# Performance work log

Hardware: AMD Instinct MI355X
Metric: run time of the kernel (lower is better)

## Reference

```python
import jax, jax.numpy as jnp
import numpy as np

B, M, D = 64, 256, 256          # batch, tokens, feature dim
A = 18                          # num_actions
E, S = 4, 64                    # num_experts, slots per expert (E*S == M)
H = 512                         # expert hidden size


def setup_inputs() -> dict:
    key = jax.random.key(0)
    ks = jax.random.split(key, 7)
    obs = jax.random.normal(ks[0], (B, M, D), dtype=jnp.float32)
    action = jax.random.randint(ks[1], (B,), 0, A, dtype=jnp.int64)
    # Soft-MoE slot projection phi: [D, E, S]
    phi = jax.random.normal(ks[2], (D, E, S), dtype=jnp.float32) / np.sqrt(D)
    # Per-expert MLP: Dense(H) + relu, then Dense(A*D) output head
    w1 = jax.random.normal(ks[3], (E, D, H), dtype=jnp.float32) * np.sqrt(2.0 / D)
    b1 = jnp.zeros((E, H), dtype=jnp.float32)
    w2 = jax.random.normal(ks[4], (E, H, A * D), dtype=jnp.float32) * np.sqrt(2.0 / H)
    b2 = jnp.zeros((E, A * D), dtype=jnp.float32)
    return {"obs": obs, "action": action, "phi": phi,
            "w1": w1, "b1": b1, "w2": w2, "b2": b2}


def reference(obs, action, phi, w1, b1, w2, b2):
    b, m, d = obs.shape
    # ---- Soft-MoE dispatch / combine (Puigcerver et al.) ----
    logits = jnp.einsum('bmd,des->bmes', obs, phi)            # [b,m,e,s]
    dispatch = jax.nn.softmax(logits, axis=1)                 # softmax over tokens
    combine = jax.nn.softmax(logits.reshape(b, m, E * S), axis=-1)
    combine = combine.reshape(b, m, E, S)                     # softmax over all slots
    slots = jnp.einsum('bmd,bmes->besd', obs, dispatch)       # [b,e,s,d]
    # ---- per-expert MLP: Dense(H)+relu -> Dense(A*d) ----
    h = jax.nn.relu(jnp.einsum('besd,edh->besh', slots, w1) + b1[None, :, None, :])
    y = jnp.einsum('besh,ehk->besk', h, w2) + b2[None, :, None, :]   # k = A*d
    # ---- combine slots back to tokens ----
    out = jnp.einsum('bmes,besk->bmk', combine, y)            # [b,m,A*d]
    # reshape to [b, A, m, d] as in the original module
    out = out.reshape(b, m, A, d).transpose(0, 2, 1, 3)       # [b,A,m,d]
    # ---- one-hot action selection via einsum (as in source) ----
    action_one_hot = jax.nn.one_hot(action, A, dtype=out.dtype)
    logits_out = jnp.einsum('bamd,ba->bmd', out, action_one_hot)
    return logits_out  # logits of the categorical transition distribution
```

## Files before the change

### kernel.cpp

```cpp
#include <hip/hip_runtime.h>

#define B_   64
#define M_   256
#define D_   256
#define A_   18
#define E_   4
#define S_   64
#define ES_  256
#define H_   512
#define K2_  (A_*D_)

typedef _Float16 f16;
typedef _Float16 f16x4 __attribute__((ext_vector_type(4)));
typedef _Float16 f16x8 __attribute__((ext_vector_type(8)));
typedef float    f32x4 __attribute__((ext_vector_type(4)));

static __device__ __forceinline__ f16x8 cat8(f16x4 a, f16x4 b) {
  return __builtin_shufflevector(a, b, 0, 1, 2, 3, 4, 5, 6, 7);
}
static __device__ __forceinline__ f16x8 pack8(float4 u0, float4 u1) {
  f16x8 a;
  a[0] = (f16)u0.x; a[1] = (f16)u0.y; a[2] = (f16)u0.z; a[3] = (f16)u0.w;
  a[4] = (f16)u1.x; a[5] = (f16)u1.y; a[6] = (f16)u1.z; a[7] = (f16)u1.w;
  return a;
}

typedef const __attribute__((address_space(1))) unsigned int guint;
typedef __attribute__((address_space(3))) unsigned int luint;
static __device__ __forceinline__ void gload16(const f16* g, f16* l) {
  __builtin_amdgcn_global_load_lds((guint*)g, (luint*)l, 16, 0, 0);
}
#define VMCNT(n)  asm volatile("s_waitcnt vmcnt(" #n ")" ::: "memory")
#define LGKMCNT0  asm volatile("s_waitcnt lgkmcnt(0)" ::: "memory")
#define SBAR()    __builtin_amdgcn_s_barrier()
#define SCHED0()  __builtin_amdgcn_sched_barrier(0)
#define MFMA16(a, b, c) __builtin_amdgcn_mfma_f32_16x16x32_f16(a, b, c, 0, 0, 0)

__global__ __launch_bounds__(256) void k_preplog(
    const float* __restrict__ obs, const float* __restrict__ phi,
    const float* __restrict__ w1, const float* __restrict__ w2,
    const int* __restrict__ action,
    f16* __restrict__ obsT16, f16* __restrict__ w1T, f16* __restrict__ w2T,
    int* __restrict__ order,
    f16* __restrict__ exp16, f16* __restrict__ expT16,
    float* __restrict__ rowpart, float* __restrict__ colpart)
{
  __shared__ f16 Bs[64][264];
  f16 (*T)[68] = reinterpret_cast<f16(*)[68]>(&Bs[0][0]);
  const int bx = blockIdx.x;
  const int t  = threadIdx.x;

  if (bx < 3456) {
    const int rr = t >> 4, cc = (t & 15) * 4;
    const float* src; f16* dst; int R, C, r0, c0;
    if (bx < 1024) {
      const int x = bx & 3, y = (bx >> 2) & 3, z = bx >> 4;
      src = obs + (long)z * (M_ * D_); dst = obsT16 + (long)z * (M_ * D_);
      R = M_; C = D_; r0 = y * 64; c0 = x * 64;
    } else if (bx < 1152) {
      const int idx = bx - 1024;
      const int x = idx & 7, y = (idx >> 3) & 3, z = idx >> 5;
      src = w1 + (long)z * (D_ * H_); dst = w1T + (long)z * (H_ * D_);
      R = D_; C = H_; r0 = y * 64; c0 = x * 64;
    } else {
      const int idx = bx - 1152;
      const int x = idx % 72, rem = idx / 72, y = rem & 7, z = rem >> 3;
      src = w2 + (long)z * ((long)H_ * K2_); dst = w2T + (long)z * ((long)K2_ * H_);
      R = H_; C = K2_; r0 = y * 64; c0 = x * 64;
    }
#pragma unroll
    for (int p = 0; p < 4; ++p) {
      const int row = rr + p * 16;
      const float4 v = *reinterpret_cast<const float4*>(
          &src[(long)(r0 + row) * C + c0 + cc]);
      f16x4 h4; h4[0] = (f16)v.x; h4[1] = (f16)v.y;
      h4[2] = (f16)v.z; h4[3] = (f16)v.w;
      *reinterpret_cast<f16x4*>(&T[row][cc]) = h4;
    }
    __syncthreads();
#pragma unroll
    for (int p = 0; p < 4; ++p) {
      const int oc = rr + p * 16;
      f16x4 g;
#pragma unroll
      for (int i = 0; i < 4; ++i) g[i] = T[cc + i][oc];
      *reinterpret_cast<f16x4*>(&dst[(long)(c0 + oc) * R + r0 + cc]) = g;
    }
    return;
  }

  if (bx == 3456) {
    if (t < B_) {
      const int a = action[t];
      int rank = 0;
#pragma unroll 8
      for (int i = 0; i < B_; ++i) {
        const int ai = action[i];
        rank += (ai < a) || (ai == a && i < t);
      }
      order[rank] = t;
    }
    return;
  }

  const int lb  = bx - 3457;
  const int es0 = (lb & 3) * 64, m0g = ((lb >> 2) & 3) * 64;
  const int bz  = lb >> 4;
  const long bo = (long)bz * (M_ * D_);
  const long bb = (long)bz * (M_ * ES_);

  {
    const int el = t & 63, wg = t >> 6;
#pragma unroll
    for (int dp = 0; dp < D_; dp += 32) {
      f16x8 hv;
#pragma unroll
      for (int j = 0; j < 8; ++j)
        hv[j] = (f16)phi[(long)(dp + wg * 8 + j) * ES_ + es0 + el];
      *reinterpret_cast<f16x8*>(&Bs[el][dp + wg * 8]) = hv;
    }
  }
  __syncthreads();

  const int w = t >> 6, lane = t & 63;
  const int wr = w >> 1, wc = w & 1;
  const int lr = lane & 15, lk = (lane >> 4) * 8;
  const int orow = (lane >> 4) * 4;

  f32x4 acc[2][2] = {};
  const float* Ap = obs + bo + (long)(m0g + wr * 32 + lr) * D_ + lk;
#pragma unroll
  for (int k0 = 0; k0 < D_; k0 += 32) {
    const float4 u00 = *reinterpret_cast<const float4*>(Ap + k0);
    const float4 u01 = *reinterpret_cast<const float4*>(Ap + k0 + 4);
    const float4 u10 = *reinterpret_cast<const float4*>(Ap + 16 * D_ + k0);
    const float4 u11 = *reinterpret_cast<const float4*>(Ap + 16 * D_ + k0 + 4);
    const f16x8 a0 = pack8(u00, u01);
    const f16x8 a1 = pack8(u10, u11);
    const f16x8 b0 = *reinterpret_cast<const f16x8*>(&Bs[wc * 32 + lr][k0 + lk]);
    const f16x8 b1 = *reinterpret_cast<const f16x8*>(&Bs[wc * 32 + 16 + lr][k0 + lk]);
    acc[0][0] = MFMA16(a0, b0, acc[0][0]);
    acc[0][1] = MFMA16(a0, b1, acc[0][1]);
    acc[1][0] = MFMA16(a1, b0, acc[1][0]);
    acc[1][1] = MFMA16(a1, b1, acc[1][1]);
  }
  __syncthreads();

#pragma unroll
  for (int fi = 0; fi < 2; ++fi)
#pragma unroll
    for (int fj = 0; fj < 2; ++fj) {
      const int gm = wr * 32 + fi * 16 + orow;
      const int gn = wc * 32 + fj * 16 + lr;
#pragma unroll
      for (int r = 0; r < 4; ++r)
        T[gm + r][gn] = (f16)__expf(acc[fi][fj][r]);
    }
  __syncthreads();

  {
    const int row = t >> 2, q = t & 3;
    f16x4 p0 = *reinterpret_cast<const f16x4*>(&T[row][q * 16 + 0]);
    f16x4 p1 = *reinterpret_cast<const f16x4*>(&T[row][q * 16 + 4]);
    f16x4 p2 = *reinterpret_cast<const f16x4*>(&T[row][q * 16 + 8]);
    f16x4 p3 = *reinterpret_cast<const f16x4*>(&T[row][q * 16 + 12]);
    f16* dst = exp16 + bb + (long)(m0g + row) * ES_ + es0 + q * 16;
    *reinterpret_cast<f16x8*>(dst)     = cat8(p0, p1);
    *reinterpret_cast<f16x8*>(dst + 8) = cat8(p2, p3);
  }
  {
    const int er = t >> 2, q = t & 3;
    f16x4 g[4];
#pragma unroll
    for (int j = 0; j < 4; ++j)
#pragma unroll
      for (int i = 0; i < 4; ++i)
        g[j][i] = T[q * 16 + j * 4 + i][er];
    f16* dst = expT16 + bb + (long)(es0 + er) * M_ + m0g + q * 16;
    *reinterpret_cast<f16x8*>(dst)     = cat8(g[0], g[1]);
    *reinterpret_cast<f16x8*>(dst + 8) = cat8(g[2], g[3]);
  }
  if (t < 64) {
    float s = 0.f;
#pragma unroll
    for (int i = 0; i < 16; ++i) {
      const f16x4 v = *reinterpret_cast<const f16x4*>(&T[t][i * 4]);
      s += (float)v[0] + (float)v[1] + (float)v[2] + (float)v[3];
    }
    rowpart[((long)bz * 256 + m0g + t) * 4 + (lb & 3)] = s;
  } else if (t < 128) {
    const int es = t - 64;
    float s = 0.f;
#pragma unroll
    for (int i = 0; i < 64; ++i) s += (float)T[i][es];
    colpart[((long)bz * 256 + es0 + es) * 4 + ((lb >> 2) & 3)] = s;
  }
}

__global__ __launch_bounds__(512, 4) void k_hy8(
    const f16* __restrict__ expT16, const f16* __restrict__ obsT16,
    const float* __restrict__ colpart,
    const f16* __restrict__ w1T, const float* __restrict__ b1,
    const f16* __restrict__ w2T, const float* __restrict__ b2,
    const int* __restrict__ action, const int* __restrict__ order,
    f16* __restrict__ yT16)
{
  __shared__ f16 lds[40960];
  f16* stg = lds;
  f16* ssO = lds + 16384;
  f16* hsO = lds + 24576;

  const int bx = blockIdx.x;
  const int L  = (bx & 7) * 64 + (bx >> 3);
  const int sb = L >> 3, e = (L >> 1) & 3, half = L & 1;
  const int b = order[sb];
  const int s0 = half * 32;
  int a = action[b];
  a = (a < 0) ? 0 : (a >= A_ ? A_ - 1 : a);

  const int t = threadIdx.x, w = t >> 6, lane = t & 63;
  const int lr = lane & 15, lk = (lane >> 4) * 8;
  const int seg = lane >> 4;
  const int orow = (lane >> 4) * 4;
  const int xorA = (lr & 7) << 3;

  const f16* srcB0 = obsT16 + (long)b * (D_ * M_);
  const f16* srcB1 = w1T + (long)e * (H_ * D_);
  const f16* srcB2 = w2T + (long)e * ((long)K2_ * H_) + (long)a * D_ * H_;
  const f16* ApG0  = expT16 + (long)b * (ES_ * M_)
                   + (long)(e * S_ + s0 + lr) * M_ + lk;

  f32x4 acc00 = {}, acc01 = {}, acc10 = {}, acc11 = {};
#pragma unroll 1
  for (int kt = 0; kt < 8; ++kt) {
    __syncthreads();
#pragma unroll
    for (int p = 0; p < 2; ++p) {
      const int j = (w * 2 + p) * 64 + lane;
      const int row = j >> 2, sg = (j & 3) ^ (row & 3);
      gload16(srcB0 + (long)row * M_ + kt * 32 + sg * 8, stg + (w * 2 + p) * 512);
    }
    __syncthreads();
    const f16x8 a0 = *reinterpret_cast<const f16x8*>(ApG0 + kt * 32);
    const f16x8 a1 = *reinterpret_cast<const f16x8*>(ApG0 + 16 * M_ + kt * 32);
    const int r0 = w * 32 + lr, r1 = w * 32 + 16 + lr;
    const f16x8 b0 = *reinterpret_cast<const f16x8*>(&stg[r0 * 32 + ((seg ^ (r0 & 3)) * 8)]);
    const f16x8 b1 = *reinterpret_cast<const f16x8*>(&stg[r1 * 32 + ((seg ^ (r1 & 3)) * 8)]);
    acc00 = MFMA16(a0, b0, acc00); acc01 = MFMA16(a0, b1, acc01);
    acc10 = MFMA16(a1, b0, acc10); acc11 = MFMA16(a1, b1, acc11);
  }
  __syncthreads();

#pragma unroll
  for (int p = 0; p < 4; ++p) {
    const int j = (w * 4 + p) * 64 + lane;
    const int row = j >> 2, sg = (j & 3) ^ (row & 3);
    gload16(srcB1 + (long)row * D_ + 0 * 32 + sg * 8, stg + (w * 4 + p) * 512);
  }
  {
    f32x4 accs[2][2] = {{acc00, acc01}, {acc10, acc11}};
    const int n0 = w * 32;
#pragma unroll
    for (int fi = 0; fi < 2; ++fi) {
      float inv[4];
#pragma unroll
      for (int r = 0; r < 4; ++r) {
        const int ges = e * S_ + s0 + fi * 16 + orow + r;
        const float4 cp = *reinterpret_cast<const float4*>(
            &colpart[((long)b * 256 + ges) * 4]);
        inv[r] = 1.0f / (cp.x + cp.y + cp.z + cp.w);
      }
#pragma unroll
      for (int fj = 0; fj < 2; ++fj) {
        const int gn = n0 + fj * 16 + lr;
#pragma unroll
        for (int r = 0; r < 4; ++r) {
          const int row = fi * 16 + orow + r;
          ssO[row * 256 + (gn ^ ((row & 7) << 3))] = (f16)(accs[fi][fj][r] * inv[r]);
        }
      }
    }
  }
#pragma unroll
  for (int p = 0; p < 4; ++p) {
    const int j = (w * 4 + p) * 64 + lane;
    const int row = j >> 2, sg = (j & 3) ^ (row & 3);
    gload16(srcB1 + (long)row * D_ + 1 * 32 + sg * 8, hsO + (w * 4 + p) * 512);
  }
  LGKMCNT0; SBAR(); SCHED0();

  f32x4 g1acc[2][4] = {};
#pragma unroll 1
  for (int kt = 0; kt < 7; ++kt) {
    VMCNT(4); SBAR(); SCHED0();
    f16* buf = (kt & 1) ? hsO : stg;
    {
      const f16x8 af0 = *reinterpret_cast<const f16x8*>(
          &ssO[lr * 256 + ((kt * 32 + lk) ^ xorA)]);
      const f16x8 af1 = *reinterpret_cast<const f16x8*>(
          &ssO[(16 + lr) * 256 + ((kt * 32 + lk) ^ xorA)]);
#pragma unroll
      for (int fj = 0; fj < 4; ++fj) {
        const int rB = w * 64 + fj * 16 + lr;
        const f16x8 bf = *reinterpret_cast<const f16x8*>(
            &buf[rB * 32 + ((seg ^ (rB & 3)) * 8)]);
        g1acc[0][fj] = MFMA16(af0, bf, g1acc[0][fj]);
        g1acc[1][fj] = MFMA16(af1, bf, g1acc[1][fj]);
      }
    }
    SBAR();
    if (kt < 6) {
#pragma unroll
      for (int p = 0; p < 4; ++p) {
        const int j = (w * 4 + p) * 64 + lane;
        const int row = j >> 2, sg = (j & 3) ^ (row & 3);
        gload16(srcB1 + (long)row * D_ + (kt + 2) * 32 + sg * 8, buf + (w * 4 + p) * 512);
      }
    }
  }
  VMCNT(0); SBAR(); SCHED0();
  {
    const f16x8 af0 = *reinterpret_cast<const f16x8*>(
        &ssO[lr * 256 + ((7 * 32 + lk) ^ xorA)]);
    const f16x8 af1 = *reinterpret_cast<const f16x8*>(
        &ssO[(16 + lr) * 256 + ((7 * 32 + lk) ^ xorA)]);
#pragma unroll
    for (int fj = 0; fj < 4; ++fj) {
      const int rB = w * 64 + fj * 16 + lr;
      const f16x8 bf = *reinterpret_cast<const f16x8*>(
          &hsO[rB * 32 + ((seg ^ (rB & 3)) * 8)]);
      g1acc[0][fj] = MFMA16(af0, bf, g1acc[0][fj]);
      g1acc[1][fj] = MFMA16(af1, bf, g1acc[1][fj]);
    }
  }
  SBAR();

#pragma unroll
  for (int p = 0; p < 2; ++p) {
    const int j = (w * 2 + p) * 64 + lane;
    const int row = j >> 2, sg = (j & 3) ^ (row & 3);
    gload16(srcB2 + (long)row * H_ + 0 * 32 + sg * 8, stg + (w * 2 + p) * 512);
  }
#pragma unroll
  for (int p = 0; p < 2; ++p) {
    const int j = (w * 2 + p) * 64 + lane;
    const int row = j >> 2, sg = (j & 3) ^ (row & 3);
    gload16(srcB2 + (long)row * H_ + 1 * 32 + sg * 8, stg + 8192 + (w * 2 + p) * 512);
  }
  {
    const int n1 = w * 64;
#pragma unroll
    for (int fi = 0; fi < 2; ++fi)
#pragma unroll
      for (int fj = 0; fj < 4; ++fj) {
        const int gn = n1 + fj * 16 + lr;
        const float bv = b1[e * H_ + gn];
#pragma unroll
        for (int r = 0; r < 4; ++r) {
          const int row = fi * 16 + orow + r;
          hsO[row * 512 + (gn ^ ((row & 7) << 3))] =
              (f16)fmaxf(g1acc[fi][fj][r] + bv, 0.f);
        }
      }
  }
  LGKMCNT0; SBAR(); SCHED0();

  f32x4 acc2[2][2] = {};
#pragma unroll 1
  for (int kt = 0; kt < 15; ++kt) {
    VMCNT(2); SBAR(); SCHED0();
    f16* buf = stg + (kt & 1) * 8192;
    {
      const f16x8 af0 = *reinterpret_cast<const f16x8*>(
          &hsO[lr * 512 + ((kt * 32 + lk) ^ xorA)]);
      const f16x8 af1 = *reinterpret_cast<const f16x8*>(
          &hsO[(16 + lr) * 512 + ((kt * 32 + lk) ^ xorA)]);
#pragma unroll
      for (int fj = 0; fj < 2; ++fj) {
        const int rB = w * 32 + fj * 16 + lr;
        const f16x8 bf = *reinterpret_cast<const f16x8*>(
            &buf[rB * 32 + ((seg ^ (rB & 3)) * 8)]);
        acc2[0][fj] = MFMA16(af0, bf, acc2[0][fj]);
        acc2[1][fj] = MFMA16(af1, bf, acc2[1][fj]);
      }
    }
    SBAR();
    if (kt < 14) {
#pragma unroll
      for (int p = 0; p < 2; ++p) {
        const int j = (w * 2 + p) * 64 + lane;
        const int row = j >> 2, sg = (j & 3) ^ (row & 3);
        gload16(srcB2 + (long)row * H_ + (kt + 2) * 32 + sg * 8, buf + (w * 2 + p) * 512);
      }
    }
  }
  VMCNT(0); SBAR(); SCHED0();
  {
    const f16x8 af0 = *reinterpret_cast<const f16x8*>(
        &hsO[lr * 512 + ((15 * 32 + lk) ^ xorA)]);
    const f16x8 af1 = *reinterpret_cast<const f16x8*>(
        &hsO[(16 + lr) * 512 + ((15 * 32 + lk) ^ xorA)]);
#pragma unroll
    for (int fj = 0; fj < 2; ++fj) {
      const int rB = w * 32 + fj * 16 + lr;
      const f16x8 bf = *reinterpret_cast<const f16x8*>(
          &stg[8192 + rB * 32 + ((seg ^ (rB & 3)) * 8)]);
      acc2[0][fj] = MFMA16(af0, bf, acc2[0][fj]);
      acc2[1][fj] = MFMA16(af1, bf, acc2[1][fj]);
    }
  }
  {
    const int n0_2 = w * 32;
#pragma unroll
    for (int fi = 0; fi < 2; ++fi)
#pragma unroll
      for (int fj = 0; fj < 2; ++fj) {
        const int gm = fi * 16 + orow;
        const int gn = n0_2 + fj * 16 + lr;
        const float bv = b2[e * K2_ + a * D_ + gn];
        f16x4 h4;
#pragma unroll
        for (int r = 0; r < 4; ++r) h4[r] = (f16)(acc2[fi][fj][r] + bv);
        *reinterpret_cast<f16x4*>(
            &yT16[(long)b * (D_ * ES_) + (long)gn * ES_ + e * S_ + s0 + gm]) = h4;
      }
  }
}

__global__ __launch_bounds__(256) void k_out_s(
    const f16* __restrict__ exp16, const f16* __restrict__ yT16,
    const float* __restrict__ rowpart, float* __restrict__ out)
{
  const int t = threadIdx.x;
  const int w = t >> 6, lane = t & 63;
  const int wr = w >> 1, wc = w & 1;
  const int m0 = blockIdx.y * 64 + wr * 32;
  const int n0 = blockIdx.x * 64 + wc * 32;
  const int lr = lane & 15, lk = (lane >> 4) * 8;
  const long b = blockIdx.z;

  f32x4 acc[2][2] = {};
  const f16* Ap = exp16 + b * (M_ * ES_) + (long)(m0 + lr) * ES_ + lk;
  const f16* Bp = yT16 + b * (D_ * ES_) + (long)(n0 + lr) * ES_ + lk;
#pragma unroll
  for (int k0 = 0; k0 < ES_; k0 += 32) {
    const f16x8 a0 = *reinterpret_cast<const f16x8*>(Ap + k0);
    const f16x8 a1 = *reinterpret_cast<const f16x8*>(Ap + 16 * ES_ + k0);
    const f16x8 b0 = *reinterpret_cast<const f16x8*>(Bp + k0);
    const f16x8 b1 = *reinterpret_cast<const f16x8*>(Bp + 16 * ES_ + k0);
    acc[0][0] = MFMA16(a0, b0, acc[0][0]);
    acc[0][1] = MFMA16(a0, b1, acc[0][1]);
    acc[1][0] = MFMA16(a1, b0, acc[1][0]);
    acc[1][1] = MFMA16(a1, b1, acc[1][1]);
  }

  const int orow = (lane >> 4) * 4;
  float* C = out + b * (M_ * D_);
#pragma unroll
  for (int fi = 0; fi < 2; ++fi) {
    float inv[4];
#pragma unroll
    for (int r = 0; r < 4; ++r) {
      const int gm = m0 + fi * 16 + orow + r;
      const float4 rp = *reinterpret_cast<const float4*>(&rowpart[((long)b * 256 + gm) * 4]);
      inv[r] = 1.0f / (rp.x + rp.y + rp.z + rp.w);
    }
#pragma unroll
    for (int fj = 0; fj < 2; ++fj) {
      const int gm = m0 + fi * 16 + orow;
      const int gn = n0 + fj * 16 + lr;
#pragma unroll
      for (int r = 0; r < 4; ++r)
        C[(long)(gm + r) * D_ + gn] = acc[fi][fj][r] * inv[r];
    }
  }
}

extern "C" void kernel_launch(void* const* d_in, const int* in_sizes, int n_in,
                              void* d_out, int out_size, void* d_ws, size_t ws_size,
                              hipStream_t stream)
{
  const float* obs    = (const float*)d_in[0];
  const int*   action = (const int*)d_in[1];
  const float* phi    = (const float*)d_in[2];
  const float* w1     = (const float*)d_in[3];
  const float* b1     = (const float*)d_in[4];
  const float* w2     = (const float*)d_in[5];
  const float* b2     = (const float*)d_in[6];
  float*       out    = (float*)d_out;

  f16* ws = (f16*)d_ws;
  f16* obsT16  = ws + 0;
  f16* w1T     = ws + 4194304;
  f16* w2T     = ws + 4718592;
  f16* exp16   = ws + 14155776;
  f16* expT16  = ws + 18350080;
  f16* yT16    = ws + 22544384;
  float* rowpart = (float*)(ws + 26738688);
  float* colpart = (float*)(ws + 26869760);
  int*   order   = (int*)(ws + 27000832);

  k_preplog<<<dim3(4481),     256, 0, stream>>>(obs, phi, w1, w2, action,
                                                obsT16, w1T, w2T, order,
                                                exp16, expT16, rowpart, colpart);
  k_hy8    <<<dim3(512),      512, 0, stream>>>(expT16, obsT16, colpart,
                                                w1T, b1, w2T, b2,
                                                action, order, yT16);
  k_out_s  <<<dim3(4, 4, 64), 256, 0, stream>>>(exp16, yT16, rowpart, out);
}
```

Baseline: 89.43 us.

## Drop block barriers in expert GEMM loops and triple-buffer the W2 stream

Each wave loads into LDS only the B-tile rows it later reads, so the per-iteration workgroup barriers in both GEMM loops of the expert MLP kernel are removed. Waves synchronise only through their own vmcnt waits. The second GEMM moves from double to triple buffering, reusing the now-idle slot staging buffer (ssO) as a third stage, so loads can be issued three k-steps ahead. This aims to cut barrier stalls and hide more global-load latency. The risk is LDS write-after-read hazards within a wave, which now depend only on waitcnt ordering.

```diff
diff --git a/kernel.cpp b/kernel.cpp
--- a/kernel.cpp
+++ b/kernel.cpp
@@ -197,7 +197,7 @@
   }
 }
 
-__global__ __launch_bounds__(512, 4) void k_hy8(
+__global__ __launch_bounds__(512, 4) void k_hy9(
     const f16* __restrict__ expT16, const f16* __restrict__ obsT16,
     const float* __restrict__ colpart,
     const f16* __restrict__ w1T, const float* __restrict__ b1,
@@ -292,7 +292,7 @@
   f32x4 g1acc[2][4] = {};
 #pragma unroll 1
   for (int kt = 0; kt < 7; ++kt) {
-    VMCNT(4); SBAR(); SCHED0();
+    VMCNT(4); SCHED0();
     f16* buf = (kt & 1) ? hsO : stg;
     {
       const f16x8 af0 = *reinterpret_cast<const f16x8*>(
@@ -308,7 +308,6 @@
         g1acc[1][fj] = MFMA16(af1, bf, g1acc[1][fj]);
       }
     }
-    SBAR();
     if (kt < 6) {
 #pragma unroll
       for (int p = 0; p < 4; ++p) {
@@ -318,7 +317,7 @@
       }
     }
   }
-  VMCNT(0); SBAR(); SCHED0();
+  VMCNT(0); SCHED0();
   {
     const f16x8 af0 = *reinterpret_cast<const f16x8*>(
         &ssO[lr * 256 + ((7 * 32 + lk) ^ xorA)]);
@@ -347,6 +346,12 @@
     const int row = j >> 2, sg = (j & 3) ^ (row & 3);
     gload16(srcB2 + (long)row * H_ + 1 * 32 + sg * 8, stg + 8192 + (w * 2 + p) * 512);
   }
+#pragma unroll
+  for (int p = 0; p < 2; ++p) {
+    const int j = (w * 2 + p) * 64 + lane;
+    const int row = j >> 2, sg = (j & 3) ^ (row & 3);
+    gload16(srcB2 + (long)row * H_ + 2 * 32 + sg * 8, ssO + (w * 2 + p) * 512);
+  }
   {
     const int n1 = w * 64;
 #pragma unroll
@@ -367,9 +372,10 @@
 
   f32x4 acc2[2][2] = {};
 #pragma unroll 1
-  for (int kt = 0; kt < 15; ++kt) {
-    VMCNT(2); SBAR(); SCHED0();
-    f16* buf = stg + (kt & 1) * 8192;
+  for (int kt = 0; kt < 13; ++kt) {
+    VMCNT(4); SCHED0();
+    const int rsel = kt % 3;
+    f16* buf = (rsel == 0) ? stg : (rsel == 1) ? (stg + 8192) : ssO;
     {
       const f16x8 af0 = *reinterpret_cast<const f16x8*>(
           &hsO[lr * 512 + ((kt * 32 + lk) ^ xorA)]);
@@ -384,27 +390,28 @@
         acc2[1][fj] = MFMA16(af1, bf, acc2[1][fj]);
       }
     }
-    SBAR();
-    if (kt < 14) {
-#pragma unroll
-      for (int p = 0; p < 2; ++p) {
-        const int j = (w * 2 + p) * 64 + lane;
-        const int row = j >> 2, sg = (j & 3) ^ (row & 3);
-        gload16(srcB2 + (long)row * H_ + (kt + 2) * 32 + sg * 8, buf + (w * 2 + p) * 512);
-      }
-    }
-  }
-  VMCNT(0); SBAR(); SCHED0();
-  {
+#pragma unroll
+    for (int p = 0; p < 2; ++p) {
+      const int j = (w * 2 + p) * 64 + lane;
+      const int row = j >> 2, sg = (j & 3) ^ (row & 3);
+      gload16(srcB2 + (long)row * H_ + (kt + 3) * 32 + sg * 8, buf + (w * 2 + p) * 512);
+    }
+  }
+#pragma unroll 1
+  for (int kt = 13; kt < 16; ++kt) {
+    if (kt == 13) { VMCNT(4); } else if (kt == 14) { VMCNT(2); } else { VMCNT(0); }
+    SCHED0();
+    const int rsel = kt % 3;
+    f16* buf = (rsel == 0) ? stg : (rsel == 1) ? (stg + 8192) : ssO;
     const f16x8 af0 = *reinterpret_cast<const f16x8*>(
-        &hsO[lr * 512 + ((15 * 32 + lk) ^ xorA)]);
+        &hsO[lr * 512 + ((kt * 32 + lk) ^ xorA)]);
     const f16x8 af1 = *reinterpret_cast<const f16x8*>(
-        &hsO[(16 + lr) * 512 + ((15 * 32 + lk) ^ xorA)]);
+        &hsO[(16 + lr) * 512 + ((kt * 32 + lk) ^ xorA)]);
 #pragma unroll
     for (int fj = 0; fj < 2; ++fj) {
       const int rB = w * 32 + fj * 16 + lr;
       const f16x8 bf = *reinterpret_cast<const f16x8*>(
-          &stg[8192 + rB * 32 + ((seg ^ (rB & 3)) * 8)]);
+          &buf[rB * 32 + ((seg ^ (rB & 3)) * 8)]);
       acc2[0][fj] = MFMA16(af0, bf, acc2[0][fj]);
       acc2[1][fj] = MFMA16(af1, bf, acc2[1][fj]);
     }
@@ -503,7 +510,7 @@
   k_preplog<<<dim3(4481),     256, 0, stream>>>(obs, phi, w1, w2, action,
                                                 obsT16, w1T, w2T, order,
                                                 exp16, expT16, rowpart, colpart);
-  k_hy8    <<<dim3(512),      512, 0, stream>>>(expT16, obsT16, colpart,
+  k_hy9    <<<dim3(512),      512, 0, stream>>>(expT16, obsT16, colpart,
                                                 w1T, b1, w2T, b2,
                                                 action, order, yT16);
   k_out_s  <<<dim3(4, 4, 64), 256, 0, stream>>>(exp16, yT16, rowpart, out);
```

Result: no change. 88.70 us (-0.8%).

## Drop w2 transpose pre-pass and stream fp32 w2 slices directly into expert GEMM

Applied to the files above, without the earlier changes.

The preprocessing kernel no longer transposes and converts all of w2 (E×H×A·D) to fp16. The second expert GEMM instead loads only the action-selected fp32 slice of w2 straight into LDS and converts it to fp16 while building MFMA operands. This removes a large full-weight read and write each call, at the cost of losing the double-buffered prefetch pipeline, reading fp32 (twice the bytes per tile) and doing strided LDS reads. Some barriers in the first GEMM loop are also removed.

```diff
diff --git a/kernel.cpp b/kernel.cpp
--- a/kernel.cpp
+++ b/kernel.cpp
@@ -27,7 +27,7 @@
 
 typedef const __attribute__((address_space(1))) unsigned int guint;
 typedef __attribute__((address_space(3))) unsigned int luint;
-static __device__ __forceinline__ void gload16(const f16* g, f16* l) {
+static __device__ __forceinline__ void gload16(const void* g, void* l) {
   __builtin_amdgcn_global_load_lds((guint*)g, (luint*)l, 16, 0, 0);
 }
 #define VMCNT(n)  asm volatile("s_waitcnt vmcnt(" #n ")" ::: "memory")
@@ -38,9 +38,8 @@
 
 __global__ __launch_bounds__(256) void k_preplog(
     const float* __restrict__ obs, const float* __restrict__ phi,
-    const float* __restrict__ w1, const float* __restrict__ w2,
-    const int* __restrict__ action,
-    f16* __restrict__ obsT16, f16* __restrict__ w1T, f16* __restrict__ w2T,
+    const float* __restrict__ w1, const int* __restrict__ action,
+    f16* __restrict__ obsT16, f16* __restrict__ w1T,
     int* __restrict__ order,
     f16* __restrict__ exp16, f16* __restrict__ expT16,
     float* __restrict__ rowpart, float* __restrict__ colpart)
@@ -50,23 +49,18 @@
   const int bx = blockIdx.x;
   const int t  = threadIdx.x;
 
-  if (bx < 3456) {
+  if (bx < 1152) {
     const int rr = t >> 4, cc = (t & 15) * 4;
     const float* src; f16* dst; int R, C, r0, c0;
     if (bx < 1024) {
       const int x = bx & 3, y = (bx >> 2) & 3, z = bx >> 4;
       src = obs + (long)z * (M_ * D_); dst = obsT16 + (long)z * (M_ * D_);
       R = M_; C = D_; r0 = y * 64; c0 = x * 64;
-    } else if (bx < 1152) {
+    } else {
       const int idx = bx - 1024;
       const int x = idx & 7, y = (idx >> 3) & 3, z = idx >> 5;
       src = w1 + (long)z * (D_ * H_); dst = w1T + (long)z * (H_ * D_);
       R = D_; C = H_; r0 = y * 64; c0 = x * 64;
-    } else {
-      const int idx = bx - 1152;
-      const int x = idx % 72, rem = idx / 72, y = rem & 7, z = rem >> 3;
-      src = w2 + (long)z * ((long)H_ * K2_); dst = w2T + (long)z * ((long)K2_ * H_);
-      R = H_; C = K2_; r0 = y * 64; c0 = x * 64;
     }
 #pragma unroll
     for (int p = 0; p < 4; ++p) {
@@ -89,7 +83,7 @@
     return;
   }
 
-  if (bx == 3456) {
+  if (bx == 1152) {
     if (t < B_) {
       const int a = action[t];
       int rank = 0;
@@ -103,7 +97,7 @@
     return;
   }
 
-  const int lb  = bx - 3457;
+  const int lb  = bx - 1153;
   const int es0 = (lb & 3) * 64, m0g = ((lb >> 2) & 3) * 64;
   const int bz  = lb >> 4;
   const long bo = (long)bz * (M_ * D_);
@@ -197,11 +191,11 @@
   }
 }
 
-__global__ __launch_bounds__(512, 4) void k_hy8(
+__global__ __launch_bounds__(512, 4) void k_hy10(
     const f16* __restrict__ expT16, const f16* __restrict__ obsT16,
     const float* __restrict__ colpart,
     const f16* __restrict__ w1T, const float* __restrict__ b1,
-    const f16* __restrict__ w2T, const float* __restrict__ b2,
+    const float* __restrict__ w2, const float* __restrict__ b2,
     const int* __restrict__ action, const int* __restrict__ order,
     f16* __restrict__ yT16)
 {
@@ -209,6 +203,7 @@
   f16* stg = lds;
   f16* ssO = lds + 16384;
   f16* hsO = lds + 24576;
+  float* stgF = reinterpret_cast<float*>(stg);
 
   const int bx = blockIdx.x;
   const int L  = (bx & 7) * 64 + (bx >> 3);
@@ -224,11 +219,11 @@
   const int orow = (lane >> 4) * 4;
   const int xorA = (lr & 7) << 3;
 
-  const f16* srcB0 = obsT16 + (long)b * (D_ * M_);
-  const f16* srcB1 = w1T + (long)e * (H_ * D_);
-  const f16* srcB2 = w2T + (long)e * ((long)K2_ * H_) + (long)a * D_ * H_;
-  const f16* ApG0  = expT16 + (long)b * (ES_ * M_)
-                   + (long)(e * S_ + s0 + lr) * M_ + lk;
+  const f16*   srcB0 = obsT16 + (long)b * (D_ * M_);
+  const f16*   srcB1 = w1T + (long)e * (H_ * D_);
+  const float* srcW2 = w2 + (long)e * ((long)H_ * K2_) + (long)a * D_;
+  const f16*   ApG0  = expT16 + (long)b * (ES_ * M_)
+                     + (long)(e * S_ + s0 + lr) * M_ + lk;
 
   f32x4 acc00 = {}, acc01 = {}, acc10 = {}, acc11 = {};
 #pragma unroll 1
@@ -292,7 +287,7 @@
   f32x4 g1acc[2][4] = {};
 #pragma unroll 1
   for (int kt = 0; kt < 7; ++kt) {
-    VMCNT(4); SBAR(); SCHED0();
+    VMCNT(4); SCHED0();
     f16* buf = (kt & 1) ? hsO : stg;
     {
       const f16x8 af0 = *reinterpret_cast<const f16x8*>(
@@ -308,7 +303,6 @@
         g1acc[1][fj] = MFMA16(af1, bf, g1acc[1][fj]);
       }
     }
-    SBAR();
     if (kt < 6) {
 #pragma unroll
       for (int p = 0; p < 4; ++p) {
@@ -318,7 +312,7 @@
       }
     }
   }
-  VMCNT(0); SBAR(); SCHED0();
+  VMCNT(0); SCHED0();
   {
     const f16x8 af0 = *reinterpret_cast<const f16x8*>(
         &ssO[lr * 256 + ((7 * 32 + lk) ^ xorA)]);
@@ -335,18 +329,6 @@
   }
   SBAR();
 
-#pragma unroll
-  for (int p = 0; p < 2; ++p) {
-    const int j = (w * 2 + p) * 64 + lane;
-    const int row = j >> 2, sg = (j & 3) ^ (row & 3);
-    gload16(srcB2 + (long)row * H_ + 0 * 32 + sg * 8, stg + (w * 2 + p) * 512);
-  }
-#pragma unroll
-  for (int p = 0; p < 2; ++p) {
-    const int j = (w * 2 + p) * 64 + lane;
-    const int row = j >> 2, sg = (j & 3) ^ (row & 3);
-    gload16(srcB2 + (long)row * H_ + 1 * 32 + sg * 8, stg + 8192 + (w * 2 + p) * 512);
-  }
   {
     const int n1 = w * 64;
 #pragma unroll
@@ -363,48 +345,30 @@
         }
       }
   }
-  LGKMCNT0; SBAR(); SCHED0();
+  __syncthreads();
 
   f32x4 acc2[2][2] = {};
 #pragma unroll 1
-  for (int kt = 0; kt < 15; ++kt) {
-    VMCNT(2); SBAR(); SCHED0();
-    f16* buf = stg + (kt & 1) * 8192;
-    {
-      const f16x8 af0 = *reinterpret_cast<const f16x8*>(
-          &hsO[lr * 512 + ((kt * 32 + lk) ^ xorA)]);
-      const f16x8 af1 = *reinterpret_cast<const f16x8*>(
-          &hsO[(16 + lr) * 512 + ((kt * 32 + lk) ^ xorA)]);
-#pragma unroll
-      for (int fj = 0; fj < 2; ++fj) {
-        const int rB = w * 32 + fj * 16 + lr;
-        const f16x8 bf = *reinterpret_cast<const f16x8*>(
-            &buf[rB * 32 + ((seg ^ (rB & 3)) * 8)]);
-        acc2[0][fj] = MFMA16(af0, bf, acc2[0][fj]);
-        acc2[1][fj] = MFMA16(af1, bf, acc2[1][fj]);
-      }
-    }
-    SBAR();
-    if (kt < 14) {
-#pragma unroll
-      for (int p = 0; p < 2; ++p) {
-        const int j = (w * 2 + p) * 64 + lane;
-        const int row = j >> 2, sg = (j & 3) ^ (row & 3);
-        gload16(srcB2 + (long)row * H_ + (kt + 2) * 32 + sg * 8, buf + (w * 2 + p) * 512);
-      }
-    }
-  }
-  VMCNT(0); SBAR(); SCHED0();
-  {
+  for (int kt = 0; kt < 16; ++kt) {
+    if (kt > 0) __syncthreads();
+#pragma unroll
+    for (int p = 0; p < 4; ++p) {
+      const int row = w * 4 + p;
+      gload16(srcW2 + ((long)(kt * 32 + row)) * K2_ + lane * 4,
+              stg + (long)row * 512);
+    }
+    __syncthreads();
     const f16x8 af0 = *reinterpret_cast<const f16x8*>(
-        &hsO[lr * 512 + ((15 * 32 + lk) ^ xorA)]);
+        &hsO[lr * 512 + ((kt * 32 + lk) ^ xorA)]);
     const f16x8 af1 = *reinterpret_cast<const f16x8*>(
-        &hsO[(16 + lr) * 512 + ((15 * 32 + lk) ^ xorA)]);
+        &hsO[(16 + lr) * 512 + ((kt * 32 + lk) ^ xorA)]);
 #pragma unroll
     for (int fj = 0; fj < 2; ++fj) {
-      const int rB = w * 32 + fj * 16 + lr;
-      const f16x8 bf = *reinterpret_cast<const f16x8*>(
-          &stg[8192 + rB * 32 + ((seg ^ (rB & 3)) * 8)]);
+      const int n = w * 32 + fj * 16 + lr;
+      f16x8 bf;
+#pragma unroll
+      for (int j = 0; j < 8; ++j)
+        bf[j] = (f16)stgF[(lk + j) * 256 + n];
       acc2[0][fj] = MFMA16(af0, bf, acc2[0][fj]);
       acc2[1][fj] = MFMA16(af1, bf, acc2[1][fj]);
     }
@@ -492,7 +456,6 @@
   f16* ws = (f16*)d_ws;
   f16* obsT16  = ws + 0;
   f16* w1T     = ws + 4194304;
-  f16* w2T     = ws + 4718592;
   f16* exp16   = ws + 14155776;
   f16* expT16  = ws + 18350080;
   f16* yT16    = ws + 22544384;
@@ -500,11 +463,11 @@
   float* colpart = (float*)(ws + 26869760);
   int*   order   = (int*)(ws + 27000832);
 
-  k_preplog<<<dim3(4481),     256, 0, stream>>>(obs, phi, w1, w2, action,
-                                                obsT16, w1T, w2T, order,
+  k_preplog<<<dim3(2177),     256, 0, stream>>>(obs, phi, w1, action,
+                                                obsT16, w1T, order,
                                                 exp16, expT16, rowpart, colpart);
-  k_hy8    <<<dim3(512),      512, 0, stream>>>(expT16, obsT16, colpart,
-                                                w1T, b1, w2T, b2,
+  k_hy10   <<<dim3(512),      512, 0, stream>>>(expT16, obsT16, colpart,
+                                                w1T, b1, w2, b2,
                                                 action, order, yT16);
   k_out_s  <<<dim3(4, 4, 64), 256, 0, stream>>>(exp16, yT16, rowpart, out);
 }
```

Measured after the change: 89.93 us. No clear change (+0.6%).
